# Optimization experiments

Measured on AMD Instinct MI355X. Metric: run time of the kernel, lower is better.

## Reference

```python
import jax, jax.numpy as jnp
import numpy as np
from jax import lax

B, C, PS, IM, P, SL = 32, 32, 256, 128, 16, 1024
DS, DC, NM = 16, 4, 2
D1, DI1, DR1 = 3 * PS, 2 * 3 * PS, 48  # mamba1: d_model=768, d_inner=1536, dt_rank=ceil(768/16)
D2, DI2, DR2 = C, 2 * C, 2              # mamba2: d_model=32,  d_inner=64,   dt_rank=ceil(32/16)
NP = (IM // P) * (IM // P)


def setup_inputs():
    ks = iter(jax.random.split(jax.random.key(0), 64))
    r = lambda *s: jax.random.normal(next(ks), s, jnp.float32) * 0.02
    inp = {
        "x_cwt": jax.random.normal(next(ks), (B, C, IM, IM), jnp.float32),
        "x_features": jax.random.normal(next(ks), (B, C, PS + SL), jnp.float32),
        "patch_conv_w": r(C, C, P, P), "patch_conv_b": r(C),
        "patch_proj_w": r(PS, NP), "patch_proj_b": r(PS),
        "feat_proj_w": r(PS // 2, SL), "feat_proj_b": r(PS // 2),
        "ln_w": jnp.ones((D1,), jnp.float32), "ln_b": jnp.zeros((D1,), jnp.float32),
        "focus": jnp.ones((1,), jnp.float32),
        "reg_w1": r(D1 // 2, D1), "reg_b1": r(D1 // 2),
        "reg_w2": r(1, D1 // 2), "reg_b2": r(1),
    }
    for tag, dm, di, dr in (("m1", D1, DI1, DR1), ("m2", D2, DI2, DR2)):
        inp[tag + "_in_w"] = r(NM, 2 * di, dm)
        inp[tag + "_conv_w"] = r(NM, di, DC)
        inp[tag + "_conv_b"] = r(NM, di)
        inp[tag + "_xp_w"] = r(NM, dr + 2 * DS, di)
        inp[tag + "_dt_w"] = r(NM, di, dr)
        inp[tag + "_dt_b"] = r(NM, di)
        inp[tag + "_A_log"] = jnp.tile(jnp.log(jnp.arange(1, DS + 1, dtype=jnp.float32)), (NM, di, 1))
        inp[tag + "_D"] = jnp.ones((NM, di), jnp.float32)
        inp[tag + "_out_w"] = r(NM, dm, di)
    return inp


def _mamba(x, in_w, conv_w, conv_b, xp_w, dt_w, dt_b, A_log, Dp, out_w):
    # x: [b, l, d_model]; standard Mamba block (in_proj -> causal dwconv -> SSM -> gate -> out_proj)
    b, l, _ = x.shape
    di, dc = conv_w.shape
    dr = dt_w.shape[1]
    ds = A_log.shape[1]
    xz = jnp.einsum('bld,ed->ble', x, in_w)
    xi, z = jnp.split(xz, 2, axis=-1)
    # causal depthwise conv1d (torch pads dc-1 both sides then truncates to l == left-pad only)
    xc = lax.conv_general_dilated(xi.transpose(0, 2, 1), conv_w[:, None, :], (1,), [(dc - 1, 0)],
                                  feature_group_count=di, dimension_numbers=('NCH', 'OIH', 'NCH'))
    xc = jax.nn.silu(xc + conv_b[None, :, None]).transpose(0, 2, 1)  # [b,l,di]
    dbl = jnp.einsum('bld,ed->ble', xc, xp_w)
    dt, Bm, Cm = dbl[..., :dr], dbl[..., dr:dr + ds], dbl[..., dr + ds:]
    delta = jax.nn.softplus(jnp.einsum('blr,dr->bld', dt, dt_w) + dt_b)
    A = -jnp.exp(A_log)                                  # [di,ds]
    dA = jnp.exp(delta[..., None] * A)                   # [b,l,di,ds]
    dBu = delta[..., None] * Bm[:, :, None, :] * xc[..., None]

    def step(h, inps):
        dA_t, dBu_t, C_t = inps
        h = dA_t * h + dBu_t
        return h, jnp.einsum('bdn,bn->bd', h, C_t)

    h0 = jnp.zeros((b, di, ds), x.dtype)
    _, ys = lax.scan(step, h0, (dA.transpose(1, 0, 2, 3), dBu.transpose(1, 0, 2, 3), Cm.transpose(1, 0, 2)))
    y = ys.transpose(1, 0, 2) + xc * Dp
    y = y * jax.nn.silu(z)
    return jnp.einsum('bld,od->blo', y, out_w)


def _stack(x, ps):
    for i in range(NM):
        x = _mamba(x, *(p[i] for p in ps)) + x
    return x


def _layernorm(x, w, b):
    mu = x.mean(-1, keepdims=True)
    v = ((x - mu) ** 2).mean(-1, keepdims=True)
    return (x - mu) * lax.rsqrt(v + 1e-5) * w + b


def reference(x_cwt, x_features, patch_conv_w, patch_conv_b, patch_proj_w, patch_proj_b,
              feat_proj_w, feat_proj_b, ln_w, ln_b, focus, reg_w1, reg_b1, reg_w2, reg_b2,
              m1_in_w, m1_conv_w, m1_conv_b, m1_xp_w, m1_dt_w, m1_dt_b, m1_A_log, m1_D, m1_out_w,
              m2_in_w, m2_conv_w, m2_conv_b, m2_xp_w, m2_dt_w, m2_dt_b, m2_A_log, m2_D, m2_out_w):
    m1 = (m1_in_w, m1_conv_w, m1_conv_b, m1_xp_w, m1_dt_w, m1_dt_b, m1_A_log, m1_D, m1_out_w)
    m2 = (m2_in_w, m2_conv_w, m2_conv_b, m2_xp_w, m2_dt_w, m2_dt_b, m2_A_log, m2_D, m2_out_w)
    # ConversionLayer: patch conv -> flatten -> linear
    xp = lax.conv_general_dilated(x_cwt, patch_conv_w, (P, P), 'VALID',
                                  dimension_numbers=('NCHW', 'OIHW', 'NCHW')) + patch_conv_b[None, :, None, None]
    x_patched = xp.reshape(x_cwt.shape[0], C, NP) @ patch_proj_w.T + patch_proj_b  # [B,C,PS]
    x_proj = jnp.concatenate([x_features[:, :, :PS // 2],
                              x_features[:, :, PS:] @ feat_proj_w.T + feat_proj_b], axis=2)  # [B,C,PS]
    x_fused = jax.nn.gelu(focus * x_proj + (2.0 - focus) * x_patched, approximate=False)
    cat = _layernorm(jnp.concatenate([x_patched, x_fused, x_proj], axis=2), ln_w, ln_b)  # [B,C,3PS]
    # mamba1 over channel axis, forward + flipped (flipped path NOT unflipped, as in source)
    x1 = _stack(cat, m1) + _stack(jnp.flip(cat, 1), m1)
    # mamba2 over feature axis
    catp = cat.transpose(0, 2, 1)  # [B,3PS,C]
    x2 = _stack(catp, m2).transpose(0, 2, 1) + _stack(jnp.flip(catp, 1), m2).transpose(0, 2, 1)
    x3 = (x1 + x2).mean(1)  # [B,3PS]
    h = x3 @ reg_w1.T + reg_b1
    return h @ reg_w2.T + reg_b2  # [B,1]
```

## Files before the change

### kernel.cpp

```cpp
#include <hip/hip_runtime.h>
#include <math.h>

#define DEV __device__ __forceinline__

DEV float sigmoid_(float x){ return 1.f/(1.f+__expf(-x)); }
DEV float silu_(float x){ return x * sigmoid_(x); }
DEV float softplus_(float x){ return (x > 20.f) ? x : log1pf(__expf(x)); }
DEV float gelu_(float x){ return 0.5f*x*(1.f + erff(x*0.70710678118654752440f)); }

typedef __attribute__((ext_vector_type(8))) short short8v;
typedef __attribute__((ext_vector_type(4))) short short4v;
typedef __attribute__((ext_vector_type(4))) float floatx4;

DEV float bfu_(unsigned short u){ return __uint_as_float(((unsigned)u) << 16); }
DEV unsigned short bfr_(float x){
  unsigned u = __float_as_uint(x);
  return (unsigned short)((u + 0x7FFFu + ((u >> 16) & 1u)) >> 16);
}
DEV short bf_split(float x, bool want_lo){
  unsigned u = __float_as_uint(x);
  unsigned hb = (u + 0x7FFFu + ((u >> 16) & 1u)) >> 16;
  if (!want_lo) return (short)hb;
  float lo = x - __uint_as_float(hb << 16);
  unsigned ul = __float_as_uint(lo);
  return (short)((ul + 0x7FFFu + ((ul >> 16) & 1u)) >> 16);
}

DEV void gl16(const short* g, short* l){
  __builtin_amdgcn_global_load_lds((const __attribute__((address_space(1))) unsigned int*)g,
                                   (__attribute__((address_space(3))) unsigned int*)l, 16, 0, 0);
}
DEV void stage64(const short* g, short* lds, int wv, int lane, int ldk){
  #pragma unroll
  for (int j = 0; j < 4; ++j){
    const int r0 = (wv << 5) + (j << 3);
    const int row = r0 + (lane >> 3);
    const int c = (lane & 7) ^ (row & 7);
    gl16(g + (size_t)row*ldk + (c << 3), lds + (r0 << 6));
  }
}
DEV int swz(int row, int cc){ return (row << 6) + (((cc) ^ (row & 7)) << 3); }

template<int ACT, int RES>
__global__ __launch_bounds__(256)
void gemm_k(const float* __restrict__ A, int lda,
            const float* __restrict__ W,
            const float* __restrict__ bias,
            const float* __restrict__ Rres,
            float* __restrict__ C, int ldc,
            int M, int N, int K)
{
  __shared__ float As[16][68];
  __shared__ float Ws[16][68];
  const int bm = blockIdx.x << 6;
  const int bn = blockIdx.y << 6;
  const int tid = threadIdx.x;
  const int tm0 = (tid >> 4) << 2;
  const int tn0 = (tid & 15) << 2;
  const int r   = tid >> 2;
  const int kk4 = (tid & 3) << 2;
  float acc[4][4] = {};
  for (int k0 = 0; k0 < K; k0 += 16) {
    const int gk = k0 + kk4;
    float4 va = make_float4(0.f,0.f,0.f,0.f);
    const int gr = bm + r;
    if (gr < M && gk < K) va = *(const float4*)(A + (size_t)gr*lda + gk);
    As[kk4+0][r]=va.x; As[kk4+1][r]=va.y; As[kk4+2][r]=va.z; As[kk4+3][r]=va.w;
    float4 vw = make_float4(0.f,0.f,0.f,0.f);
    const int gc = bn + r;
    if (gc < N && gk < K) vw = *(const float4*)(W + (size_t)gc*K + gk);
    Ws[kk4+0][r]=vw.x; Ws[kk4+1][r]=vw.y; Ws[kk4+2][r]=vw.z; Ws[kk4+3][r]=vw.w;
    __syncthreads();
    #pragma unroll
    for (int kk = 0; kk < 16; ++kk) {
      const float a0=As[kk][tm0+0], a1=As[kk][tm0+1], a2=As[kk][tm0+2], a3=As[kk][tm0+3];
      const float w0=Ws[kk][tn0+0], w1=Ws[kk][tn0+1], w2=Ws[kk][tn0+2], w3=Ws[kk][tn0+3];
      acc[0][0]+=a0*w0; acc[0][1]+=a0*w1; acc[0][2]+=a0*w2; acc[0][3]+=a0*w3;
      acc[1][0]+=a1*w0; acc[1][1]+=a1*w1; acc[1][2]+=a1*w2; acc[1][3]+=a1*w3;
      acc[2][0]+=a2*w0; acc[2][1]+=a2*w1; acc[2][2]+=a2*w2; acc[2][3]+=a2*w3;
      acc[3][0]+=a3*w0; acc[3][1]+=a3*w1; acc[3][2]+=a3*w2; acc[3][3]+=a3*w3;
    }
    __syncthreads();
  }
  #pragma unroll
  for (int i=0;i<4;i++){
    const int row = bm + tm0 + i;
    if (row >= M) continue;
    #pragma unroll
    for (int j=0;j<4;j++){
      const int col = bn + tn0 + j;
      if (col >= N) continue;
      float v = acc[i][j];
      if (bias) v += bias[col];
      if (RES)  v += Rres[(size_t)row*ldc + col];
      if (ACT == 1) v = softplus_(v);
      C[(size_t)row*ldc + col] = v;
    }
  }
}

template<int C, int KP, int MODE>
__global__ void cvt3t_k(const float* __restrict__ X, int ldx, short* __restrict__ Y,
                        int realR, int total4)
{
  const int i4 = blockIdx.x*256 + threadIdx.x;
  if (i4 >= total4) return;
  const int idx = i4 << 2;
  const int c3 = idx % KP;
  const int r  = idx / KP;
  short4v out = {0,0,0,0};
  const int nparts = (MODE == 2) ? 2 : 3;
  if (r < realR && c3 < nparts*C) {
    const int part = c3 / C;
    const int c = c3 - part*C;
    const bool lo = (MODE == 1) ? (part == 2) : (part == 1);
    const float4 v = *(const float4*)(X + (size_t)r*ldx + c);
    out.x = bf_split(v.x, lo); out.y = bf_split(v.y, lo);
    out.z = bf_split(v.z, lo); out.w = bf_split(v.w, lo);
  }
  *(short4v*)(Y + (size_t)r*KP + c3) = out;
}

template<int ACT, int RES, int BIAS>
__global__ __launch_bounds__(256)
void gemm3g_k(const short* __restrict__ A3, const short* __restrict__ W3,
              const float* __restrict__ bias, const float* __restrict__ Rres,
              float* __restrict__ C, int ldc, int NOUT, int M, int K3)
{
  __shared__ __align__(16) short As[128*64];
  __shared__ __align__(16) short Ws[128*64];
  const int tid = threadIdx.x;
  const int lane = tid & 63;
  const int wv = tid >> 6;
  const int bm = blockIdx.x << 7;
  const int bn = blockIdx.y << 7;
  const int wr = (wv >> 1) << 6;
  const int wc = (wv & 1) << 6;
  const int frow = lane & 15;
  const int fk = lane >> 4;
  floatx4 acc[4][4] = {};
  const short* gA = A3 + (size_t)bm*K3;
  const short* gW = W3 + (size_t)bn*K3;
  for (int k0 = 0; k0 < K3; k0 += 64) {
    __syncthreads();
    stage64(gA + k0, As, wv, lane, K3);
    stage64(gW + k0, Ws, wv, lane, K3);
    __syncthreads();
    #pragma unroll
    for (int kk = 0; kk < 2; ++kk) {
      short8v af[4], bfv[4];
      #pragma unroll
      for (int mf = 0; mf < 4; ++mf)
        af[mf] = *(const short8v*)&As[swz(wr + mf*16 + frow, kk*4 + fk)];
      #pragma unroll
      for (int nf = 0; nf < 4; ++nf)
        bfv[nf] = *(const short8v*)&Ws[swz(wc + nf*16 + frow, kk*4 + fk)];
      #pragma unroll
      for (int mf = 0; mf < 4; ++mf)
        #pragma unroll
        for (int nf = 0; nf < 4; ++nf)
          acc[mf][nf] = __builtin_amdgcn_mfma_f32_16x16x32_bf16(af[mf], bfv[nf], acc[mf][nf], 0, 0, 0);
    }
  }
  #pragma unroll
  for (int mf = 0; mf < 4; ++mf) {
    #pragma unroll
    for (int nf = 0; nf < 4; ++nf) {
      const int col = bn + wc + nf*16 + (lane & 15);
      if (col >= NOUT) continue;
      #pragma unroll
      for (int r = 0; r < 4; ++r) {
        const int row = bm + wr + mf*16 + (lane >> 4)*4 + r;
        float v = acc[mf][nf][r];
        if (BIAS) v += bias[col];
        if (RES)  v += Rres[(size_t)row*ldc + col];
        if (ACT == 1) v = softplus_(v);
        C[(size_t)row*ldc + col] = v;
      }
    }
  }
}

__global__ __launch_bounds__(256)
void gemm3gd_k(const short* __restrict__ A2, const short* __restrict__ W2,
               float* __restrict__ C, int ldc, int M, int K)
{
  __shared__ __align__(16) short Ash[128*64];
  __shared__ __align__(16) short Asl[128*64];
  __shared__ __align__(16) short Wsh[128*64];
  __shared__ __align__(16) short Wsl[128*64];
  const int tid = threadIdx.x;
  const int lane = tid & 63;
  const int wv = tid >> 6;
  const int bm = blockIdx.x << 7;
  const int bn = blockIdx.y << 7;
  const int wr = (wv >> 1) << 6;
  const int wc = (wv & 1) << 6;
  const int frow = lane & 15;
  const int fk = lane >> 4;
  floatx4 acc[4][4] = {};
  const short* gA = A2 + (size_t)bm*(2*K);
  const short* gW = W2 + (size_t)bn*(2*K);
  for (int k0 = 0; k0 < K; k0 += 64) {
    __syncthreads();
    stage64(gA + k0,     Ash, wv, lane, 2*K);
    stage64(gA + k0 + K, Asl, wv, lane, 2*K);
    stage64(gW + k0,     Wsh, wv, lane, 2*K);
    stage64(gW + k0 + K, Wsl, wv, lane, 2*K);
    __syncthreads();
    #pragma unroll
    for (int kk = 0; kk < 2; ++kk) {
      short8v ah[4], bh[4];
      #pragma unroll
      for (int mf = 0; mf < 4; ++mf)
        ah[mf] = *(const short8v*)&Ash[swz(wr + mf*16 + frow, kk*4 + fk)];
      #pragma unroll
      for (int nf = 0; nf < 4; ++nf)
        bh[nf] = *(const short8v*)&Wsh[swz(wc + nf*16 + frow, kk*4 + fk)];
      #pragma unroll
      for (int mf = 0; mf < 4; ++mf)
        #pragma unroll
        for (int nf = 0; nf < 4; ++nf)
          acc[mf][nf] = __builtin_amdgcn_mfma_f32_16x16x32_bf16(ah[mf], bh[nf], acc[mf][nf], 0, 0, 0);
      #pragma unroll
      for (int nf = 0; nf < 4; ++nf) {
        const short8v bl = *(const short8v*)&Wsl[swz(wc + nf*16 + frow, kk*4 + fk)];
        #pragma unroll
        for (int mf = 0; mf < 4; ++mf)
          acc[mf][nf] = __builtin_amdgcn_mfma_f32_16x16x32_bf16(ah[mf], bl, acc[mf][nf], 0, 0, 0);
      }
      #pragma unroll
      for (int mf = 0; mf < 4; ++mf) {
        const short8v al = *(const short8v*)&Asl[swz(wr + mf*16 + frow, kk*4 + fk)];
        #pragma unroll
        for (int nf = 0; nf < 4; ++nf)
          acc[mf][nf] = __builtin_amdgcn_mfma_f32_16x16x32_bf16(al, bh[nf], acc[mf][nf], 0, 0, 0);
      }
    }
  }
  #pragma unroll
  for (int mf = 0; mf < 4; ++mf) {
    #pragma unroll
    for (int nf = 0; nf < 4; ++nf) {
      const int col = bn + wc + nf*16 + (lane & 15);
      #pragma unroll
      for (int r = 0; r < 4; ++r) {
        const int row = bm + wr + mf*16 + (lane >> 4)*4 + r;
        C[(size_t)row*ldc + col] = acc[mf][nf][r];
      }
    }
  }
}

__global__ __launch_bounds__(256)
void gemm3gz_k(const short* __restrict__ A3, const short* __restrict__ W3,
               float* __restrict__ C, int ldc, int NOUT, int M, int K3, int KC)
{
  __shared__ __align__(16) short As[128*64];
  __shared__ __align__(16) short Ws[128*64];
  const int tid = threadIdx.x;
  const int lane = tid & 63;
  const int wv = tid >> 6;
  const int bm = blockIdx.x << 7;
  const int bn = blockIdx.y << 7;
  const int kbeg = blockIdx.z * KC;
  float* Cpart = C + (size_t)blockIdx.z * M * ldc;
  const int wr = (wv >> 1) << 6;
  const int wc = (wv & 1) << 6;
  const int frow = lane & 15;
  const int fk = lane >> 4;
  floatx4 acc[4][4] = {};
  const short* gA = A3 + (size_t)bm*K3 + kbeg;
  const short* gW = W3 + (size_t)bn*K3 + kbeg;
  for (int k0 = 0; k0 < KC; k0 += 64) {
    __syncthreads();
    stage64(gA + k0, As, wv, lane, K3);
    stage64(gW + k0, Ws, wv, lane, K3);
    __syncthreads();
    #pragma unroll
    for (int kk = 0; kk < 2; ++kk) {
      short8v af[4], bfv[4];
      #pragma unroll
      for (int mf = 0; mf < 4; ++mf)
        af[mf] = *(const short8v*)&As[swz(wr + mf*16 + frow, kk*4 + fk)];
      #pragma unroll
      for (int nf = 0; nf < 4; ++nf)
        bfv[nf] = *(const short8v*)&Ws[swz(wc + nf*16 + frow, kk*4 + fk)];
      #pragma unroll
      for (int mf = 0; mf < 4; ++mf)
        #pragma unroll
        for (int nf = 0; nf < 4; ++nf)
          acc[mf][nf] = __builtin_amdgcn_mfma_f32_16x16x32_bf16(af[mf], bfv[nf], acc[mf][nf], 0, 0, 0);
    }
  }
  #pragma unroll
  for (int mf = 0; mf < 4; ++mf) {
    #pragma unroll
    for (int nf = 0; nf < 4; ++nf) {
      const int col = bn + wc + nf*16 + (lane & 15);
      if (col >= NOUT) continue;
      #pragma unroll
      for (int r = 0; r < 4; ++r) {
        const int row = bm + wr + mf*16 + (lane >> 4)*4 + r;
        Cpart[(size_t)row*ldc + col] = acc[mf][nf][r];
      }
    }
  }
}

__global__ __launch_bounds__(256)
void gemm3gd32_k(const short* __restrict__ A2, const short* __restrict__ W2,
                 float* __restrict__ C, int M, int K, int KC)
{
  __shared__ __align__(16) short Ash[128*64];
  __shared__ __align__(16) short Asl[128*64];
  __shared__ __align__(16) short Wsh[32*64];
  __shared__ __align__(16) short Wsl[32*64];
  const int tid = threadIdx.x;
  const int lane = tid & 63;
  const int wv = tid >> 6;
  const int bm = blockIdx.x << 7;
  const int kbeg = blockIdx.z * KC;
  float* Cpart = C + (size_t)blockIdx.z * M * 32;
  const int wr = wv << 5;
  const int frow = lane & 15;
  const int fk = lane >> 4;
  floatx4 acc[2][2] = {};
  const short* gA = A2 + (size_t)bm*(2*K) + kbeg;
  const short* gW = W2 + kbeg;
  for (int k0 = 0; k0 < KC; k0 += 64) {
    __syncthreads();
    stage64(gA + k0,     Ash, wv, lane, 2*K);
    stage64(gA + k0 + K, Asl, wv, lane, 2*K);
    {
      const int r0 = wv << 3;
      const int row = r0 + (lane >> 3);
      const int c = (lane & 7) ^ (row & 7);
      gl16(gW + k0 +     (size_t)row*(2*K) + (c << 3), Wsh + (r0 << 6));
      gl16(gW + k0 + K + (size_t)row*(2*K) + (c << 3), Wsl + (r0 << 6));
    }
    __syncthreads();
    #pragma unroll
    for (int kk = 0; kk < 2; ++kk) {
      short8v ah[2], al[2], bh[2], blv[2];
      #pragma unroll
      for (int mf = 0; mf < 2; ++mf) {
        ah[mf] = *(const short8v*)&Ash[swz(wr + mf*16 + frow, kk*4 + fk)];
        al[mf] = *(const short8v*)&Asl[swz(wr + mf*16 + frow, kk*4 + fk)];
      }
      #pragma unroll
      for (int nf = 0; nf < 2; ++nf) {
        bh[nf]  = *(const short8v*)&Wsh[swz(nf*16 + frow, kk*4 + fk)];
        blv[nf] = *(const short8v*)&Wsl[swz(nf*16 + frow, kk*4 + fk)];
      }
      #pragma unroll
      for (int mf = 0; mf < 2; ++mf)
        #pragma unroll
        for (int nf = 0; nf < 2; ++nf) {
          acc[mf][nf] = __builtin_amdgcn_mfma_f32_16x16x32_bf16(ah[mf], bh[nf],  acc[mf][nf], 0, 0, 0);
          acc[mf][nf] = __builtin_amdgcn_mfma_f32_16x16x32_bf16(ah[mf], blv[nf], acc[mf][nf], 0, 0, 0);
          acc[mf][nf] = __builtin_amdgcn_mfma_f32_16x16x32_bf16(al[mf], bh[nf],  acc[mf][nf], 0, 0, 0);
        }
    }
  }
  #pragma unroll
  for (int mf = 0; mf < 2; ++mf) {
    #pragma unroll
    for (int nf = 0; nf < 2; ++nf) {
      const int col = nf*16 + (lane & 15);
      #pragma unroll
      for (int r = 0; r < 4; ++r) {
        const int row = bm + wr + mf*16 + (lane >> 4)*4 + r;
        Cpart[(size_t)row*32 + col] = acc[mf][nf][r];
      }
    }
  }
}

__global__ __launch_bounds__(256)
void gemm3gz2_k(const short* __restrict__ A2, const short* __restrict__ W2,
                float* __restrict__ C0, float* __restrict__ C1,
                int ldc, int NOUT, int M, int K, int KC)
{
  __shared__ __align__(16) short As[128*64];
  __shared__ __align__(16) short Ws[128*64];
  const int tid = threadIdx.x;
  const int lane = tid & 63;
  const int wv = tid >> 6;
  const int bm = blockIdx.x << 7;
  const int bn = blockIdx.y << 7;
  const int z = blockIdx.z;
  const int pp = z >> 1;
  const int ks = z & 1;
  const int kA = ((pp == 2) ? K : 0) + ks*KC;
  const int kW = ((pp == 1) ? K : 0) + ks*KC;
  float* Cpart = (z < 4) ? (C0 + (size_t)z * M * ldc) : (C1 + (size_t)(z-4) * M * ldc);
  const int wr = (wv >> 1) << 6;
  const int wc = (wv & 1) << 6;
  const int frow = lane & 15;
  const int fk = lane >> 4;
  floatx4 acc[4][4] = {};
  const short* gA = A2 + (size_t)bm*(2*K) + kA;
  const short* gW = W2 + (size_t)bn*(2*K) + kW;
  for (int k0 = 0; k0 < KC; k0 += 64) {
    __syncthreads();
    stage64(gA + k0, As, wv, lane, 2*K);
    stage64(gW + k0, Ws, wv, lane, 2*K);
    __syncthreads();
    #pragma unroll
    for (int kk = 0; kk < 2; ++kk) {
      short8v af[4], bfv[4];
      #pragma unroll
      for (int mf = 0; mf < 4; ++mf)
        af[mf] = *(const short8v*)&As[swz(wr + mf*16 + frow, kk*4 + fk)];
      #pragma unroll
      for (int nf = 0; nf < 4; ++nf)
        bfv[nf] = *(const short8v*)&Ws[swz(wc + nf*16 + frow, kk*4 + fk)];
      #pragma unroll
      for (int mf = 0; mf < 4; ++mf)
        #pragma unroll
        for (int nf = 0; nf < 4; ++nf)
          acc[mf][nf] = __builtin_amdgcn_mfma_f32_16x16x32_bf16(af[mf], bfv[nf], acc[mf][nf], 0, 0, 0);
    }
  }
  #pragma unroll
  for (int mf = 0; mf < 4; ++mf) {
    #pragma unroll
    for (int nf = 0; nf < 4; ++nf) {
      const int col = bn + wc + nf*16 + (lane & 15);
      if (col >= NOUT) continue;
      #pragma unroll
      for (int r = 0; r < 4; ++r) {
        const int row = bm + wr + mf*16 + (lane >> 4)*4 + r;
        Cpart[(size_t)row*ldc + col] = acc[mf][nf][r];
      }
    }
  }
}

__global__ void reduce_xp_k(const float* __restrict__ part, float* __restrict__ out)
{
  const int i = blockIdx.x*256 + threadIdx.x;
  if (i >= 163840) return;
  float s = 0.f;
  #pragma unroll
  for (int z = 0; z < 8; ++z) s += part[(size_t)z*163840 + i];
  out[i] = s;
}
__global__ void reduce_feat_k(const float* __restrict__ part, const float* __restrict__ bias,
                              float* __restrict__ out)
{
  const int i = blockIdx.x*256 + threadIdx.x;
  if (i >= 131072) return;
  const int r = i >> 7, c = i & 127;
  float s = bias[c];
  #pragma unroll
  for (int z = 0; z < 8; ++z) s += part[(size_t)z*131072 + i];
  out[(size_t)r*256 + 128 + c] = s;
}
template<int EMIT>
__global__ void reduce_out_k(const float* __restrict__ p0, const float* __restrict__ p1,
                             float* __restrict__ m1x, short* __restrict__ A2i)
{
  const int i = blockIdx.x*256 + threadIdx.x;
  if (i >= 1572864) return;
  float s = m1x[i];
  #pragma unroll
  for (int z = 0; z < 4; ++z) s += p0[(size_t)z*1572864 + i];
  #pragma unroll
  for (int z = 0; z < 2; ++z) s += p1[(size_t)z*1572864 + i];
  m1x[i] = s;
  if (EMIT) {
    const int d = i % 768;
    const int sl = i / 768;
    const short hi = bf_split(s,false), lo = bf_split(s,true);
    short* p = A2i + (size_t)sl*1536 + d;
    p[0] = hi; p[768] = lo;
  }
}

__global__ __launch_bounds__(256)
void dt1_k(const float* __restrict__ dbl, const float* __restrict__ dt_w,
           const float* __restrict__ dt_b, float* __restrict__ delta)
{
  const int d = blockIdx.y*256 + threadIdx.x;
  const int r0 = blockIdx.x*8;
  float w[48];
  #pragma unroll
  for (int q = 0; q < 12; ++q)
    *(float4*)&w[q*4] = *(const float4*)(dt_w + (size_t)d*48 + q*4);
  __shared__ float sdbl[8][48];
  if (threadIdx.x < 96) {
    const int rr = threadIdx.x / 12, q = threadIdx.x % 12;
    *(float4*)&sdbl[rr][q*4] = *(const float4*)(dbl + (size_t)(r0+rr)*80 + q*4);
  }
  __syncthreads();
  const float bv = dt_b[d];
  #pragma unroll
  for (int rr = 0; rr < 8; ++rr) {
    float acc = bv;
    #pragma unroll
    for (int k = 0; k < 48; ++k) acc += sdbl[rr][k]*w[k];
    delta[(size_t)(r0+rr)*1536 + d] = softplus_(acc);
  }
}

__global__ void im2col2_k(const float* __restrict__ x, int c0, short* __restrict__ A2)
{
  const int t = blockIdx.x*256 + threadIdx.x;
  if (t >= 2097152) return;
  const int b = t >> 16;
  const int r = t & 65535;
  const int c = r >> 12;
  const int f = r & 4095;
  const float4 v = *(const float4*)(x + (((size_t)b*32 + c0 + c) << 14) + (f << 2));
  const int o4 = f << 2;
  const int h = o4 >> 7, w = o4 & 127;
  const int patch = ((h >> 4) << 3) + (w >> 4);
  const int pos = ((h & 15) << 4) + (w & 15);
  const int row = (b << 6) + patch;
  const int k = (c << 8) + pos;
  short4v hv, lv;
  hv.x = bf_split(v.x,false); lv.x = bf_split(v.x,true);
  hv.y = bf_split(v.y,false); lv.y = bf_split(v.y,true);
  hv.z = bf_split(v.z,false); lv.z = bf_split(v.z,true);
  hv.w = bf_split(v.w,false); lv.w = bf_split(v.w,true);
  short* base = A2 + (size_t)row*8192 + k;
  *(short4v*)(base)        = hv;
  *(short4v*)(base + 4096) = lv;
}

__global__ void reduce_patch16_k(const float* __restrict__ part, const float* __restrict__ bias,
                                 short* __restrict__ A3p)
{
  const int idx = blockIdx.x*256 + threadIdx.x;
  if (idx >= 65536) return;
  const int patch = idx & 63;
  const int o = (idx >> 6) & 31;
  const int b = idx >> 11;
  const int row = (b << 6) + patch;
  float s = bias[o];
  #pragma unroll
  for (int z = 0; z < 32; ++z) s += part[(size_t)z*65536 + row*32 + o];
  const short hi = bf_split(s,false), lo = bf_split(s,true);
  short* p = A3p + (size_t)((b << 5) + o)*192 + patch;
  p[0] = hi; p[64] = hi; p[128] = lo;
}

__global__ __launch_bounds__(256)
void fuse_ln_k(const float* __restrict__ xpat, const float* __restrict__ xprojbuf,
               const float* __restrict__ xfeat, const float* __restrict__ lnw,
               const float* __restrict__ lnb, const float* __restrict__ focusp,
               float* __restrict__ cat)
{
  const int row = blockIdx.x;
  const int t = threadIdx.x;
  const float focus = focusp[0];
  const float xp = xpat[(size_t)row*256 + t];
  const float pr = (t < 128) ? xfeat[(size_t)row*1280 + t] : xprojbuf[(size_t)row*256 + t];
  const float xf = gelu_(focus*pr + (2.f - focus)*xp);
  float s  = xp + xf + pr;
  float sq = xp*xp + xf*xf + pr*pr;
  __shared__ float rs[4], rq[4];
  const int lane = t & 63, wv = t >> 6;
  #pragma unroll
  for (int off = 32; off > 0; off >>= 1) {
    s  += __shfl_down(s,  off, 64);
    sq += __shfl_down(sq, off, 64);
  }
  if (lane == 0) { rs[wv] = s; rq[wv] = sq; }
  __syncthreads();
  const float S = rs[0]+rs[1]+rs[2]+rs[3];
  const float Q = rq[0]+rq[1]+rq[2]+rq[3];
  const float mu = S * (1.f/768.f);
  const float var = Q*(1.f/768.f) - mu*mu;
  const float rstd = rsqrtf(var + 1e-5f);
  const size_t ob = (size_t)row*768;
  cat[ob +        t] = (xp - mu)*rstd*lnw[      t] + lnb[      t];
  cat[ob + 256 +  t] = (xf - mu)*rstd*lnw[256 + t] + lnb[256 + t];
  cat[ob + 512 +  t] = (pr - mu)*rstd*lnw[512 + t] + lnb[512 + t];
}

__global__ void prep_m1_k(const float* __restrict__ cat, float* __restrict__ X,
                          short* __restrict__ A2i)
{
  const int idx = blockIdx.x*256 + threadIdx.x;
  if (idx >= 64*32*768) return;
  const int d = idx % 768;
  const int sl = idx / 768;
  const int l = sl & 31;
  const int s = sl >> 5;
  const int b = s & 31;
  const int ll = (s < 32) ? l : 31 - l;
  const float v = cat[((size_t)b*32 + ll)*768 + d];
  X[idx] = v;
  const short hi = bf_split(v,false), lo = bf_split(v,true);
  short* p = A2i + (size_t)sl*1536 + d;
  p[0] = hi; p[768] = lo;
}
__global__ void prep_m2_k(const float* __restrict__ cat, float* __restrict__ X)
{
  const int idx = blockIdx.x*256 + threadIdx.x;
  if (idx >= 64*768*32) return;
  const int c = idx & 31;
  const int sj = idx >> 5;
  const int j = sj % 768;
  const int s = sj / 768;
  const int b = (s < 32) ? s : s - 32;
  const int jj = (s < 32) ? j : 767 - j;
  X[idx] = cat[((size_t)b*32 + c)*768 + jj];
}

__global__ void dwconv_silu_k(const float* __restrict__ xz, int ldxz,
                              const float* __restrict__ w, const float* __restrict__ b,
                              float* __restrict__ xc, int di, int L, int total)
{
  const int idx = blockIdx.x*256 + threadIdx.x;
  if (idx >= total) return;
  const int d = idx % di;
  const int sl = idx / di;
  const int l = sl % L;
  float acc = b[d];
  const float* wd = w + d*4;
  #pragma unroll
  for (int k = 0; k < 4; ++k) {
    const int ll = l - 3 + k;
    if (ll >= 0) acc += xz[(size_t)(sl - 3 + k)*ldxz + d] * wd[k];
  }
  xc[idx] = silu_(acc);
}

__global__ void dwconv3_m1_k(const float* __restrict__ xz,
                             const float* __restrict__ w, const float* __restrict__ b,
                             float* __restrict__ xc, short* __restrict__ A3x)
{
  const int idx = blockIdx.x*256 + threadIdx.x;
  if (idx >= 3145728) return;
  const int d = idx % 1536;
  const int sl = idx / 1536;
  const int l = sl & 31;
  float acc = b[d];
  const float* wd = w + d*4;
  #pragma unroll
  for (int k = 0; k < 4; ++k) {
    const int ll = l - 3 + k;
    if (ll >= 0) acc += xz[(size_t)(sl - 3 + k)*3072 + d] * wd[k];
  }
  const float v = silu_(acc);
  xc[idx] = v;
  const short hi = bf_split(v,false), lo = bf_split(v,true);
  short* p = A3x + (size_t)sl*4608 + d;
  p[0] = hi; p[1536] = hi; p[3072] = lo;
}

__global__ void dt2_k(const float* __restrict__ dbl, const float* __restrict__ dt_w,
                      const float* __restrict__ dt_b, float* __restrict__ delta)
{
  const int idx = blockIdx.x*256 + threadIdx.x;
  if (idx >= 49152*64) return;
  const int d = idx & 63;
  const int r = idx >> 6;
  const float a0 = dbl[(size_t)r*34 + 0], a1 = dbl[(size_t)r*34 + 1];
  delta[idx] = softplus_(a0*dt_w[d*2] + a1*dt_w[d*2+1] + dt_b[d]);
}

__global__ __launch_bounds__(256)
void scan3s_m1_k(const float* __restrict__ delta, const float* __restrict__ xc,
                 const float* __restrict__ dbl, const float* __restrict__ z,
                 const float* __restrict__ A_log, const float* __restrict__ Dp,
                 short* __restrict__ A3o)
{
  const int s = blockIdx.x / 24;
  const int dchunk = blockIdx.x % 24;
  const int lane = threadIdx.x & 63;
  const int wv = threadIdx.x >> 6;
  const int d = dchunk*64 + wv*16 + (lane & 15);
  const int hf = lane >> 4;
  const int n0 = hf*4;
  float A[4], h[4];
  #pragma unroll
  for (int n = 0; n < 4; ++n) { A[n] = -__expf(A_log[d*16 + n0 + n]); h[n] = 0.f; }
  const float Dv = Dp[d];
  for (int l = 0; l < 32; ++l) {
    const size_t row = (size_t)s*32 + l;
    const float de  = delta[row*1536 + d];
    const float xcv = xc[row*1536 + d];
    const float du  = de * xcv;
    const float* bl = dbl + row*80 + 48 + n0;
    float y = 0.f;
    #pragma unroll
    for (int n = 0; n < 4; ++n) {
      const float dA = __expf(de * A[n]);
      h[n] = dA*h[n] + du*bl[n];
      y += h[n]*bl[16 + n];
    }
    y += __shfl_xor(y, 16);
    y += __shfl_xor(y, 32);
    if (hf == 0) {
      const float zv = z[row*3072 + d];
      const float out = (y + xcv*Dv) * silu_(zv);
      short* p = A3o + row*3072 + d;
      p[0] = bf_split(out,false);
      p[1536] = bf_split(out,true);
    }
  }
}

#define NC2 24
#define LC2 32

__global__ __launch_bounds__(256)
void scan2_partA(const float* __restrict__ delta, const float* __restrict__ xc,
                 const float* __restrict__ dbl, const float* __restrict__ A_log,
                 unsigned short* __restrict__ Hend, unsigned short* __restrict__ sde_buf)
{
  const int s = blockIdx.x / NC2;
  const int c = blockIdx.x % NC2;
  const int lane = threadIdx.x & 63;
  const int wv = threadIdx.x >> 6;
  const int d = wv*16 + (lane & 15);
  const int hf = lane >> 4;
  const int n0 = hf*4;
  float A[4], h[4];
  #pragma unroll
  for (int n = 0; n < 4; ++n) { A[n] = -__expf(A_log[d*16 + n0 + n]); h[n] = 0.f; }
  float sde = 0.f;
  const size_t row0 = (size_t)s*768 + c*LC2;
  for (int l = 0; l < LC2; ++l) {
    const size_t row = row0 + l;
    const float de  = delta[row*64 + d];
    const float xcv = xc[row*64 + d];
    const float du  = de * xcv;
    const float* bl = dbl + row*34 + 2 + n0;
    sde += de;
    #pragma unroll
    for (int n = 0; n < 4; ++n)
      h[n] = __expf(de*A[n])*h[n] + du*bl[n];
  }
  short4v hv;
  hv.x = (short)bfr_(h[0]); hv.y = (short)bfr_(h[1]);
  hv.z = (short)bfr_(h[2]); hv.w = (short)bfr_(h[3]);
  *(short4v*)(Hend + ((size_t)((s*NC2 + c)*64 + d))*16 + n0) = hv;
  if (hf == 0) sde_buf[(s*NC2 + c)*64 + d] = bfr_(sde);
}

__global__ void scan2_carry(const float* __restrict__ A_log,
                            unsigned short* __restrict__ Hend,
                            const unsigned short* __restrict__ sde_buf)
{
  const int t = blockIdx.x*256 + threadIdx.x;
  if (t >= 4096) return;
  const int d = t & 63;
  const int s = t >> 6;
  float A[16], H[16];
  #pragma unroll
  for (int n = 0; n < 16; ++n) { A[n] = -__expf(A_log[d*16 + n]); H[n] = 0.f; }
  for (int c = 0; c < NC2; ++c) {
    const size_t off = ((size_t)(s*NC2 + c)*64 + d)*16;
    const float sde = bfu_(sde_buf[(s*NC2 + c)*64 + d]);
    #pragma unroll
    for (int n = 0; n < 16; ++n) {
      const float he = bfu_(Hend[off + n]);
      Hend[off + n] = bfr_(H[n]);
      H[n] = __expf(sde*A[n])*H[n] + he;
    }
  }
}

__global__ __launch_bounds__(256)
void scan2_partC(const float* __restrict__ delta, const float* __restrict__ xc,
                 const float* __restrict__ dbl, const float* __restrict__ z,
                 const float* __restrict__ A_log, const float* __restrict__ Dp,
                 const unsigned short* __restrict__ Hin, float* __restrict__ Y)
{
  const int s = blockIdx.x / NC2;
  const int c = blockIdx.x % NC2;
  const int lane = threadIdx.x & 63;
  const int wv = threadIdx.x >> 6;
  const int d = wv*16 + (lane & 15);
  const int hf = lane >> 4;
  const int n0 = hf*4;
  float A[4], h[4];
  const unsigned short* hp = Hin + ((size_t)((s*NC2 + c)*64 + d))*16 + n0;
  #pragma unroll
  for (int n = 0; n < 4; ++n) {
    A[n] = -__expf(A_log[d*16 + n0 + n]);
    h[n] = bfu_(hp[n]);
  }
  const float Dv = Dp[d];
  const size_t row0 = (size_t)s*768 + c*LC2;
  for (int l = 0; l < LC2; ++l) {
    const size_t row = row0 + l;
    const float de  = delta[row*64 + d];
    const float xcv = xc[row*64 + d];
    const float du  = de * xcv;
    const float* bl = dbl + row*34 + 2 + n0;
    float y = 0.f;
    #pragma unroll
    for (int n = 0; n < 4; ++n) {
      const float dA = __expf(de*A[n]);
      h[n] = dA*h[n] + du*bl[n];
      y += h[n]*bl[16 + n];
    }
    y += __shfl_xor(y, 16);
    y += __shfl_xor(y, 32);
    if (hf == 0) {
      const float zv = z[row*128 + d];
      Y[row*64 + d] = (y + xcv*Dv) * silu_(zv);
    }
  }
}

__global__ __launch_bounds__(256)
void x3_k(const float* __restrict__ x1p, const float* __restrict__ x2p, float* __restrict__ x3)
{
  const int b = blockIdx.x / 24;
  const int jc = blockIdx.x % 24;
  const int jl = threadIdx.x & 31;
  const int ig = threadIdx.x >> 5;
  const int j = jc*32 + jl;
  float s = 0.f;
  #pragma unroll
  for (int q = 0; q < 4; ++q) {
    const int i = ig*4 + q;
    s += x1p[((size_t)b*32 + i)*768 + j] + x1p[((size_t)(b+32)*32 + i)*768 + j];
    s += x2p[((size_t)b*768 + j)*32 + i] + x2p[((size_t)(b+32)*768 + j)*32 + i];
  }
  __shared__ float red[8][33];
  red[ig][jl] = s;
  __syncthreads();
  if (ig == 0) {
    float t = 0.f;
    #pragma unroll
    for (int g = 0; g < 8; ++g) t += red[g][jl];
    x3[(size_t)b*768 + j] = t * (1.f/32.f);
  }
}

__global__ __launch_bounds__(256)
void head1_k(const float* __restrict__ x3, const float* __restrict__ w1,
             const float* __restrict__ b1, const float* __restrict__ w2,
             float* __restrict__ h)
{
  const int b = blockIdx.x;
  const int lane = threadIdx.x & 63;
  const int wv = threadIdx.x >> 6;
  const int t = blockIdx.y*4 + wv;
  float dot = 0.f;
  const float* xr = x3 + (size_t)b*768;
  const float* wr = w1 + (size_t)t*768;
  #pragma unroll
  for (int k = 0; k < 12; ++k)
    dot += xr[lane + k*64] * wr[lane + k*64];
  #pragma unroll
  for (int off = 32; off > 0; off >>= 1) dot += __shfl_down(dot, off, 64);
  if (lane == 0) h[(size_t)b*384 + t] = (dot + b1[t]) * w2[t];
}

__global__ __launch_bounds__(64)
void head2_k(const float* __restrict__ h, const float* __restrict__ b2,
             float* __restrict__ out)
{
  const int b = blockIdx.x;
  const int lane = threadIdx.x;
  float s = 0.f;
  #pragma unroll
  for (int k = 0; k < 6; ++k) s += h[(size_t)b*384 + k*64 + lane];
  #pragma unroll
  for (int off = 32; off > 0; off >>= 1) s += __shfl_down(s, off, 64);
  if (lane == 0) out[b] = s + b2[0];
}

extern "C" void kernel_launch(void* const* d_in, const int* in_sizes, int n_in,
                              void* d_out, int out_size, void* d_ws, size_t ws_size,
                              hipStream_t stream)
{
  (void)in_sizes; (void)n_in; (void)out_size;
  const float* x_cwt        = (const float*)d_in[0];
  const float* x_features   = (const float*)d_in[1];
  const float* patch_conv_w = (const float*)d_in[2];
  const float* patch_conv_b = (const float*)d_in[3];
  const float* patch_proj_w = (const float*)d_in[4];
  const float* patch_proj_b = (const float*)d_in[5];
  const float* feat_proj_w  = (const float*)d_in[6];
  const float* feat_proj_b  = (const float*)d_in[7];
  const float* ln_w         = (const float*)d_in[8];
  const float* ln_b         = (const float*)d_in[9];
  const float* focus        = (const float*)d_in[10];
  const float* reg_w1       = (const float*)d_in[11];
  const float* reg_b1       = (const float*)d_in[12];
  const float* reg_w2       = (const float*)d_in[13];
  const float* reg_b2       = (const float*)d_in[14];
  const float* m1w[9]; for (int i=0;i<9;i++) m1w[i] = (const float*)d_in[15+i];
  const float* m2w[9]; for (int i=0;i<9;i++) m2w[i] = (const float*)d_in[24+i];

  float* p = (float*)d_ws;
  size_t need = 0;
  auto alloc = [&](size_t n){ float* r = p; p += n; need += n; return r; };
  float* cat    = alloc(786432);
  float* m1x    = alloc(1572864);
  float* m2x    = alloc(1572864);
  float* x3     = alloc(24576);
  float* bxz    = alloc(6291456);
  float* bxc    = alloc(3145728);
  float* bdbl   = alloc(1671168);
  float* bdelta = alloc(3145728);
  float* by     = alloc(3145728);
  if (ws_size < need * sizeof(float)) return;

  short* A2pc  = (short*)bxz;
  short* W2pc  = (short*)by;
  float* pcpart = by + 800000;
  float* x_patched = m1x;
  float* x_projb   = m1x + 262144;
  short* A3p = (short*)(m1x + 524288);
  short* W3p = (short*)(m1x + 630016);
  short* A3f = (short*)bxz;
  short* W3f = (short*)(bxz + 1600000);
  float* featpart = m2x;
  short* A2i  = (short*)bxc;
  short* W2i  = (short*)bdbl;
  short* A3x  = (short*)bdbl;
  short* W3x  = (short*)by;
  float* xppart = m2x;
  short* A3o  = (short*)by;
  short* W3o  = (short*)bxc;
  float* outp0 = bxz;
  float* outp1 = bdelta;
  unsigned short* sHend = (unsigned short*)cat;
  unsigned short* sSde  = (unsigned short*)x3;
  float* hbuf = bxz;

  im2col2_k<<<8192, 256, 0, stream>>>(x_cwt, 0, A2pc);
  cvt3t_k<4096,8192,2><<<256, 256, 0, stream>>>(patch_conv_w, 8192, W2pc, 32, 65536);
  gemm3gd32_k<<<dim3(16,1,16), 256, 0, stream>>>(A2pc, W2pc, pcpart, 2048, 4096, 256);
  im2col2_k<<<8192, 256, 0, stream>>>(x_cwt, 16, A2pc);
  cvt3t_k<4096,8192,2><<<256, 256, 0, stream>>>(patch_conv_w + 4096, 8192, W2pc, 32, 65536);
  gemm3gd32_k<<<dim3(16,1,16), 256, 0, stream>>>(A2pc, W2pc, pcpart + 16*65536, 2048, 4096, 256);
  reduce_patch16_k<<<256, 256, 0, stream>>>(pcpart, patch_conv_b, A3p);
  cvt3t_k<64,192,0><<<48, 256, 0, stream>>>(patch_proj_w, 64, W3p, 256, 12288);
  gemm3g_k<0,0,1><<<dim3(8,2), 256, 0, stream>>>(A3p, W3p, patch_proj_b, nullptr,
                                                 x_patched, 256, 256, 1024, 192);
  cvt3t_k<1024,3072,1><<<3072, 256, 0, stream>>>(x_features + 256, 1280, A3f, 1024, 786432);
  cvt3t_k<1024,3072,0><<<384, 256, 0, stream>>>(feat_proj_w, 1024, W3f, 128, 98304);
  gemm3gz_k<<<dim3(8,1,8), 256, 0, stream>>>(A3f, W3f, featpart, 128, 128, 1024, 3072, 384);
  reduce_feat_k<<<512, 256, 0, stream>>>(featpart, feat_proj_b, x_projb);
  fuse_ln_k<<<1024, 256, 0, stream>>>(x_patched, x_projb, x_features, ln_w, ln_b, focus, cat);
  prep_m1_k<<<6144, 256, 0, stream>>>(cat, m1x, A2i);

  for (int im = 0; im < 2; ++im) {
    const float* in_w   = m1w[0] + (size_t)im*3072*768;
    const float* conv_w = m1w[1] + (size_t)im*1536*4;
    const float* conv_b = m1w[2] + (size_t)im*1536;
    const float* xp_w   = m1w[3] + (size_t)im*80*1536;
    const float* dt_w   = m1w[4] + (size_t)im*1536*48;
    const float* dt_b   = m1w[5] + (size_t)im*1536;
    const float* A_log  = m1w[6] + (size_t)im*1536*16;
    const float* Dp     = m1w[7] + (size_t)im*1536;
    const float* out_w  = m1w[8] + (size_t)im*768*1536;
    cvt3t_k<768,1536,2><<<4608, 256, 0, stream>>>(in_w, 768, W2i, 3072, 1179648);
    gemm3gd_k<<<dim3(16,24), 256, 0, stream>>>(A2i, W2i, bxz, 3072, 2048, 768);
    dwconv3_m1_k<<<12288, 256, 0, stream>>>(bxz, conv_w, conv_b, bxc, A3x);
    cvt3t_k<1536,4608,0><<<576, 256, 0, stream>>>(xp_w, 1536, W3x, 80, 147456);
    gemm3gz_k<<<dim3(16,1,8), 256, 0, stream>>>(A3x, W3x, xppart, 80, 80, 2048, 4608, 576);
    reduce_xp_k<<<640, 256, 0, stream>>>(xppart, bdbl);
    dt1_k<<<dim3(256,6), 256, 0, stream>>>(bdbl, dt_w, dt_b, bdelta);
    scan3s_m1_k<<<1536, 256, 0, stream>>>(bdelta, bxc, bdbl, bxz + 1536, A_log, Dp, A3o);
    cvt3t_k<1536,3072,2><<<2304, 256, 0, stream>>>(out_w, 1536, W3o, 768, 589824);
    gemm3gz2_k<<<dim3(16,6,6), 256, 0, stream>>>(A3o, W3o, outp0, outp1, 768, 768, 2048, 1536, 768);
    if (im == 0) reduce_out_k<1><<<6144, 256, 0, stream>>>(outp0, outp1, m1x, A2i);
    else         reduce_out_k<0><<<6144, 256, 0, stream>>>(outp0, outp1, m1x, nullptr);
  }

  prep_m2_k<<<6144, 256, 0, stream>>>(cat, m2x);

  for (int im = 0; im < 2; ++im) {
    const float* in_w   = m2w[0] + (size_t)im*128*32;
    const float* conv_w = m2w[1] + (size_t)im*64*4;
    const float* conv_b = m2w[2] + (size_t)im*64;
    const float* xp_w   = m2w[3] + (size_t)im*34*64;
    const float* dt_w   = m2w[4] + (size_t)im*64*2;
    const float* dt_b   = m2w[5] + (size_t)im*64;
    const float* A_log  = m2w[6] + (size_t)im*64*16;
    const float* Dp     = m2w[7] + (size_t)im*64;
    const float* out_w  = m2w[8] + (size_t)im*32*64;
    gemm_k<0,0><<<dim3(768,2), 256, 0, stream>>>(m2x, 32, in_w, nullptr, nullptr,
                                                 bxz, 128, 49152, 128, 32);
    dwconv_silu_k<<<12288, 256, 0, stream>>>(bxz, 128, conv_w, conv_b, bxc, 64, 768, 49152*64);
    gemm_k<0,0><<<dim3(768,1), 256, 0, stream>>>(bxc, 64, xp_w, nullptr, nullptr,
                                                 bdbl, 34, 49152, 34, 64);
    dt2_k<<<12288, 256, 0, stream>>>(bdbl, dt_w, dt_b, bdelta);
    scan2_partA<<<1536, 256, 0, stream>>>(bdelta, bxc, bdbl, A_log, sHend, sSde);
    scan2_carry<<<16, 256, 0, stream>>>(A_log, sHend, sSde);
    scan2_partC<<<1536, 256, 0, stream>>>(bdelta, bxc, bdbl, bxz + 64, A_log, Dp, sHend, by);
    gemm_k<0,1><<<dim3(768,1), 256, 0, stream>>>(by, 64, out_w, nullptr, m2x,
                                                 m2x, 32, 49152, 32, 64);
  }

  x3_k<<<768, 256, 0, stream>>>(m1x, m2x, x3);
  head1_k<<<dim3(32,96), 256, 0, stream>>>(x3, reg_w1, reg_b1, reg_w2, hbuf);
  head2_k<<<32, 64, 0, stream>>>(hbuf, reg_b2, (float*)d_out);
}
```

Baseline: 735.6 us.

## Fuse bf16 hi/lo split-GEMM terms into one kernel for mamba1 out_proj

The mamba1 out_proj used to launch separate split-K blocks for each of the three bf16x3 product terms (hi*hi, hi*lo, lo*hi) and write six partial planes. The new kernel stages the hi and lo tiles of A and W together and accumulates all three products in one accumulator. It uses a 3-way K split, so only three partial planes are written and reduced. This cuts partial-sum global traffic and reuses each staged tile across the products, at the cost of doubled shared memory per block (64KB) and fewer blocks in flight.

```diff
diff --git a/kernel.cpp b/kernel.cpp
--- a/kernel.cpp
+++ b/kernel.cpp
@@ -253,6 +253,79 @@
 }
 
 __global__ __launch_bounds__(256)
+void gemm3gdz_k(const short* __restrict__ A2, const short* __restrict__ W2,
+                float* __restrict__ C, int ldc, int M, int K, int KC)
+{
+  __shared__ __align__(16) short Ash[128*64];
+  __shared__ __align__(16) short Asl[128*64];
+  __shared__ __align__(16) short Wsh[128*64];
+  __shared__ __align__(16) short Wsl[128*64];
+  const int tid = threadIdx.x;
+  const int lane = tid & 63;
+  const int wv = tid >> 6;
+  const int bm = blockIdx.x << 7;
+  const int bn = blockIdx.y << 7;
+  const int kbeg = blockIdx.z * KC;
+  float* Cpart = C + (size_t)blockIdx.z * M * ldc;
+  const int wr = (wv >> 1) << 6;
+  const int wc = (wv & 1) << 6;
+  const int frow = lane & 15;
+  const int fk = lane >> 4;
+  floatx4 acc[4][4] = {};
+  const short* gA = A2 + (size_t)bm*(2*K) + kbeg;
+  const short* gW = W2 + (size_t)bn*(2*K) + kbeg;
+  for (int k0 = 0; k0 < KC; k0 += 64) {
+    __syncthreads();
+    stage64(gA + k0,     Ash, wv, lane, 2*K);
+    stage64(gA + k0 + K, Asl, wv, lane, 2*K);
+    stage64(gW + k0,     Wsh, wv, lane, 2*K);
+    stage64(gW + k0 + K, Wsl, wv, lane, 2*K);
+    __syncthreads();
+    #pragma unroll
+    for (int kk = 0; kk < 2; ++kk) {
+      short8v ah[4], bh[4];
+      #pragma unroll
+      for (int mf = 0; mf < 4; ++mf)
+        ah[mf] = *(const short8v*)&Ash[swz(wr + mf*16 + frow, kk*4 + fk)];
+      #pragma unroll
+      for (int nf = 0; nf < 4; ++nf)
+        bh[nf] = *(const short8v*)&Wsh[swz(wc + nf*16 + frow, kk*4 + fk)];
+      #pragma unroll
+      for (int mf = 0; mf < 4; ++mf)
+        #pragma unroll
+        for (int nf = 0; nf < 4; ++nf)
+          acc[mf][nf] = __builtin_amdgcn_mfma_f32_16x16x32_bf16(ah[mf], bh[nf], acc[mf][nf], 0, 0, 0);
+      #pragma unroll
+      for (int nf = 0; nf < 4; ++nf) {
+        const short8v bl = *(const short8v*)&Wsl[swz(wc + nf*16 + frow, kk*4 + fk)];
+        #pragma unroll
+        for (int mf = 0; mf < 4; ++mf)
+          acc[mf][nf] = __builtin_amdgcn_mfma_f32_16x16x32_bf16(ah[mf], bl, acc[mf][nf], 0, 0, 0);
+      }
+      #pragma unroll
+      for (int mf = 0; mf < 4; ++mf) {
+        const short8v al = *(const short8v*)&Asl[swz(wr + mf*16 + frow, kk*4 + fk)];
+        #pragma unroll
+        for (int nf = 0; nf < 4; ++nf)
+          acc[mf][nf] = __builtin_amdgcn_mfma_f32_16x16x32_bf16(al, bh[nf], acc[mf][nf], 0, 0, 0);
+      }
+    }
+  }
+  #pragma unroll
+  for (int mf = 0; mf < 4; ++mf) {
+    #pragma unroll
+    for (int nf = 0; nf < 4; ++nf) {
+      const int col = bn + wc + nf*16 + (lane & 15);
+      #pragma unroll
+      for (int r = 0; r < 4; ++r) {
+        const int row = bm + wr + mf*16 + (lane >> 4)*4 + r;
+        Cpart[(size_t)row*ldc + col] = acc[mf][nf][r];
+      }
+    }
+  }
+}
+
+__global__ __launch_bounds__(256)
 void gemm3gz_k(const short* __restrict__ A3, const short* __restrict__ W3,
                float* __restrict__ C, int ldc, int NOUT, int M, int K3, int KC)
 {
@@ -377,67 +450,6 @@
   }
 }
 
-__global__ __launch_bounds__(256)
-void gemm3gz2_k(const short* __restrict__ A2, const short* __restrict__ W2,
-                float* __restrict__ C0, float* __restrict__ C1,
-                int ldc, int NOUT, int M, int K, int KC)
-{
-  __shared__ __align__(16) short As[128*64];
-  __shared__ __align__(16) short Ws[128*64];
-  const int tid = threadIdx.x;
-  const int lane = tid & 63;
-  const int wv = tid >> 6;
-  const int bm = blockIdx.x << 7;
-  const int bn = blockIdx.y << 7;
-  const int z = blockIdx.z;
-  const int pp = z >> 1;
-  const int ks = z & 1;
-  const int kA = ((pp == 2) ? K : 0) + ks*KC;
-  const int kW = ((pp == 1) ? K : 0) + ks*KC;
-  float* Cpart = (z < 4) ? (C0 + (size_t)z * M * ldc) : (C1 + (size_t)(z-4) * M * ldc);
-  const int wr = (wv >> 1) << 6;
-  const int wc = (wv & 1) << 6;
-  const int frow = lane & 15;
-  const int fk = lane >> 4;
-  floatx4 acc[4][4] = {};
-  const short* gA = A2 + (size_t)bm*(2*K) + kA;
-  const short* gW = W2 + (size_t)bn*(2*K) + kW;
-  for (int k0 = 0; k0 < KC; k0 += 64) {
-    __syncthreads();
-    stage64(gA + k0, As, wv, lane, 2*K);
-    stage64(gW + k0, Ws, wv, lane, 2*K);
-    __syncthreads();
-    #pragma unroll
-    for (int kk = 0; kk < 2; ++kk) {
-      short8v af[4], bfv[4];
-      #pragma unroll
-      for (int mf = 0; mf < 4; ++mf)
-        af[mf] = *(const short8v*)&As[swz(wr + mf*16 + frow, kk*4 + fk)];
-      #pragma unroll
-      for (int nf = 0; nf < 4; ++nf)
-        bfv[nf] = *(const short8v*)&Ws[swz(wc + nf*16 + frow, kk*4 + fk)];
-      #pragma unroll
-      for (int mf = 0; mf < 4; ++mf)
-        #pragma unroll
-        for (int nf = 0; nf < 4; ++nf)
-          acc[mf][nf] = __builtin_amdgcn_mfma_f32_16x16x32_bf16(af[mf], bfv[nf], acc[mf][nf], 0, 0, 0);
-    }
-  }
-  #pragma unroll
-  for (int mf = 0; mf < 4; ++mf) {
-    #pragma unroll
-    for (int nf = 0; nf < 4; ++nf) {
-      const int col = bn + wc + nf*16 + (lane & 15);
-      if (col >= NOUT) continue;
-      #pragma unroll
-      for (int r = 0; r < 4; ++r) {
-        const int row = bm + wr + mf*16 + (lane >> 4)*4 + r;
-        Cpart[(size_t)row*ldc + col] = acc[mf][nf][r];
-      }
-    }
-  }
-}
-
 __global__ void reduce_xp_k(const float* __restrict__ part, float* __restrict__ out)
 {
   const int i = blockIdx.x*256 + threadIdx.x;
@@ -459,16 +471,14 @@
   out[(size_t)r*256 + 128 + c] = s;
 }
 template<int EMIT>
-__global__ void reduce_out_k(const float* __restrict__ p0, const float* __restrict__ p1,
-                             float* __restrict__ m1x, short* __restrict__ A2i)
+__global__ void reduce_out3_k(const float* __restrict__ p0, float* __restrict__ m1x,
+                              short* __restrict__ A2i)
 {
   const int i = blockIdx.x*256 + threadIdx.x;
   if (i >= 1572864) return;
   float s = m1x[i];
   #pragma unroll
-  for (int z = 0; z < 4; ++z) s += p0[(size_t)z*1572864 + i];
-  #pragma unroll
-  for (int z = 0; z < 2; ++z) s += p1[(size_t)z*1572864 + i];
+  for (int z = 0; z < 3; ++z) s += p0[(size_t)z*1572864 + i];
   m1x[i] = s;
   if (EMIT) {
     const int d = i % 768;
@@ -926,7 +936,6 @@
   short* A3o  = (short*)by;
   short* W3o  = (short*)bxc;
   float* outp0 = bxz;
-  float* outp1 = bdelta;
   unsigned short* sHend = (unsigned short*)cat;
   unsigned short* sSde  = (unsigned short*)x3;
   float* hbuf = bxz;
@@ -967,9 +976,9 @@
     dt1_k<<<dim3(256,6), 256, 0, stream>>>(bdbl, dt_w, dt_b, bdelta);
     scan3s_m1_k<<<1536, 256, 0, stream>>>(bdelta, bxc, bdbl, bxz + 1536, A_log, Dp, A3o);
     cvt3t_k<1536,3072,2><<<2304, 256, 0, stream>>>(out_w, 1536, W3o, 768, 589824);
-    gemm3gz2_k<<<dim3(16,6,6), 256, 0, stream>>>(A3o, W3o, outp0, outp1, 768, 768, 2048, 1536, 768);
-    if (im == 0) reduce_out_k<1><<<6144, 256, 0, stream>>>(outp0, outp1, m1x, A2i);
-    else         reduce_out_k<0><<<6144, 256, 0, stream>>>(outp0, outp1, m1x, nullptr);
+    gemm3gdz_k<<<dim3(16,6,3), 256, 0, stream>>>(A3o, W3o, outp0, 768, 2048, 1536, 512);
+    if (im == 0) reduce_out3_k<1><<<6144, 256, 0, stream>>>(outp0, m1x, A2i);
+    else         reduce_out3_k<0><<<6144, 256, 0, stream>>>(outp0, m1x, nullptr);
   }
 
   prep_m2_k<<<6144, 256, 0, stream>>>(cat, m2x);
```

Measured after the change: 691.9 us. 6.0% less time.
